# Optimization experiments

Measured on AMD Instinct MI355X. Metric: run time of the kernel, lower is better.

Reference implementation:

```python
import jax, jax.numpy as jnp
import numpy as np

B, N, E = 16, 2048, 256


def setup_inputs() -> dict:
    key = jax.random.key(0)
    ks = jax.random.split(key, 9)
    locs = jax.random.uniform(ks[0], (B, N, 2), dtype=jnp.float32)
    probe = jax.random.randint(ks[1], (B, N), 0, 2).astype(bool)
    probe = probe.at[:, 0].set(True)  # guarantee >=1 probe per instance
    s = 0.02
    W_node = jax.random.normal(ks[2], (2, E), dtype=jnp.float32) * s
    b_node = jax.random.normal(ks[3], (E,), dtype=jnp.float32) * s
    W_dist = jax.random.normal(ks[4], (1, E), dtype=jnp.float32) * s
    b_dist = jax.random.normal(ks[5], (E,), dtype=jnp.float32) * s
    W_out = jax.random.normal(ks[6], (2 * E, E), dtype=jnp.float32) * s
    b_out = jax.random.normal(ks[7], (E,), dtype=jnp.float32) * s
    return {
        "locs": locs, "probe": probe,
        "W_node": W_node, "b_node": b_node,
        "W_dist": W_dist, "b_dist": b_dist,
        "W_out": W_out, "b_out": b_out,
    }


def _cdist(x):
    # pairwise euclidean distance [B,N,N] with safe sqrt (0-grad at 0)
    sq = jnp.sum(x * x, axis=-1)                       # [B,N]
    d2 = sq[:, :, None] + sq[:, None, :] - 2.0 * jnp.einsum("bnd,bmd->bnm", x, x)
    d2 = jnp.maximum(d2, 0.0)
    pos = d2 > 0.0
    return jnp.where(pos, jnp.sqrt(jnp.where(pos, d2, 1.0)), 0.0)


def reference(locs, probe, W_node, b_node, W_dist, b_dist, W_out, b_out):
    node_emb = locs @ W_node + b_node                  # [B,N,E]
    dist = _cdist(locs)                                # [B,N,N]
    # rows i that are NOT probes are set to +inf, then min over rows (dim=1)
    dist = jnp.where(probe[:, :, None], dist, jnp.inf)
    min_dist = jnp.min(dist, axis=1)                   # [B,N] dist to nearest probe
    dist_emb = min_dist[..., None] @ W_dist + b_dist   # [B,N,E]
    cat = jnp.concatenate([node_emb, dist_emb], axis=-1)
    return cat @ W_out + b_out                         # [B,N,E]
```

## Files before the change

kernel.cpp:

```cpp
#include <hip/hip_runtime.h>

#define BSZ  16
#define NPTS 2048
#define EDIM 256
#define QB   64
#define FPB  16


__global__ __launch_bounds__(256) void prep(
    const float* __restrict__ Wn,
    const float* __restrict__ bn,
    const float* __restrict__ Wd,
    const float* __restrict__ bd,
    const float* __restrict__ Wo,
    const float* __restrict__ locs,
    const int*   __restrict__ probe,
    float*  __restrict__ partials,
    int*    __restrict__ gcnt,
    float2* __restrict__ glist)
{
    __shared__ int cnt;
    const int t   = threadIdx.x;
    const int blk = blockIdx.x;

    if (blk < FPB) {
        const int e = t;
        float a = 0.f, b = 0.f, c = 0.f, d = 0.f;
#pragma unroll
        for (int kk = 0; kk < EDIM / FPB; ++kk) {
            const int k = blk * (EDIM / FPB) + kk;
            const float wt = Wo[k * EDIM + e];
            const float wb = Wo[(EDIM + k) * EDIM + e];
            a = fmaf(Wn[k],        wt, a);
            b = fmaf(Wn[EDIM + k], wt, b);
            d = fmaf(bn[k],        wt, d);
            c = fmaf(Wd[k],        wb, c);
            d = fmaf(bd[k],        wb, d);
        }
        float* o = partials + blk * 4 * EDIM;
        o[0 * EDIM + e] = a;
        o[1 * EDIM + e] = b;
        o[2 * EDIM + e] = c;
        o[3 * EDIM + e] = d;
    } else {
        const int b = blk - FPB;
        if (t == 0) cnt = 0;
        __syncthreads();
        const float2* lb = reinterpret_cast<const float2*>(locs) + (size_t)b * NPTS;
        float2* gl = glist + (size_t)b * NPTS;
        const int lane = t & 63;
#pragma unroll
        for (int jj = 0; jj < NPTS / 256; ++jj) {
            const int j = jj * 256 + t;
            const float2 p = lb[j];
            const bool pred = probe[b * NPTS + j] != 0;
            const unsigned long long mb = __ballot(pred);
            const int rank = __popcll(mb & ((1ull << lane) - 1ull));
            int base = 0;
            if (lane == 0) base = atomicAdd(&cnt, __popcll(mb));
            base = __shfl(base, 0);
            if (pred) gl[base + rank] = p;
        }
        __syncthreads();
        if (t == 0) gcnt[b] = cnt;
    }
}

__global__ __launch_bounds__(256) void mdpp_main(
    const float*  __restrict__ locs,
    const float*  __restrict__ partials,
    const int*    __restrict__ gcnt,
    const float2* __restrict__ glist,
    const float*  __restrict__ bo,
    float*        __restrict__ out)
{
    __shared__ __align__(16) float2 pl[NPTS + 32];
    __shared__ float folded[4 * EDIM];
    __shared__ float partmin[16][QB];
    __shared__ float xq[QB], yq[QB], dq[QB];

    const int t    = threadIdx.x;
    const int bid  = blockIdx.x;
    const int b    = bid >> 5;
    const int n0   = (bid & 31) * QB;
    const int lane = t & 63;
    const int w    = t >> 6;

    const int M  = gcnt[b];
    const int Mp = (M + 31) & ~31;

    const float2* gl = glist + (size_t)b * NPTS;
    for (int i = t; i < M; i += 256) pl[i] = gl[i];
    if (t < Mp - M) pl[M + t] = make_float2(1.0e19f, 1.0e19f);

#pragma unroll
    for (int v = 0; v < 4; ++v) {
        float s = 0.f;
#pragma unroll
        for (int p = 0; p < FPB; ++p) s += partials[p * 4 * EDIM + v * EDIM + t];
        if (v == 3) s += bo[t];
        folded[v * EDIM + t] = s;
    }

    if (t < QB) {
        const float2 p = reinterpret_cast<const float2*>(locs)[(size_t)b * NPTS + n0 + t];
        xq[t] = p.x;
        yq[t] = p.y;
    }
    __syncthreads();

    const int qb    = lane & 15;
    const int chunk = w * 4 + (lane >> 4);
    float qx[4], qy[4], best[4];
#pragma unroll
    for (int j = 0; j < 4; ++j) {
        qx[j] = xq[j * 16 + qb];
        qy[j] = yq[j * 16 + qb];
        best[j] = 3.0e38f;
    }
    const int S2 = Mp >> 5;
    const float4* pl4 = reinterpret_cast<const float4*>(pl);
    const int lo = chunk * S2, hi = lo + S2;
#pragma unroll 2
    for (int i = lo; i < hi; ++i) {
        const float4 pp = pl4[i];
#pragma unroll
        for (int j = 0; j < 4; ++j) {
            const float dx0 = qx[j] - pp.x, dy0 = qy[j] - pp.y;
            const float dx1 = qx[j] - pp.z, dy1 = qy[j] - pp.w;
            best[j] = fminf(best[j], fmaf(dy0, dy0, dx0 * dx0));
            best[j] = fminf(best[j], fmaf(dy1, dy1, dx1 * dx1));
        }
    }
#pragma unroll
    for (int j = 0; j < 4; ++j) partmin[chunk][j * 16 + qb] = best[j];
    __syncthreads();

    if (t < QB) {
        float m = partmin[0][t];
#pragma unroll
        for (int c = 1; c < 16; ++c) m = fminf(m, partmin[c][t]);
        dq[t] = sqrtf(m);
    }
    __syncthreads();

    const int e0 = lane * 4;
    float A[4], Bv[4], C[4], D[4];
#pragma unroll
    for (int i = 0; i < 4; ++i) {
        A[i]  = folded[0 * EDIM + e0 + i];
        Bv[i] = folded[1 * EDIM + e0 + i];
        C[i]  = folded[2 * EDIM + e0 + i];
        D[i]  = folded[3 * EDIM + e0 + i];
    }
#pragma unroll
    for (int it = 0; it < 16; ++it) {
        const int r = it * 4 + w;
        const float xx = xq[r], yy = yq[r], dd = dq[r];
        float4 st;
        st.x = fmaf(xx, A[0], fmaf(yy, Bv[0], fmaf(dd, C[0], D[0])));
        st.y = fmaf(xx, A[1], fmaf(yy, Bv[1], fmaf(dd, C[1], D[1])));
        st.z = fmaf(xx, A[2], fmaf(yy, Bv[2], fmaf(dd, C[2], D[2])));
        st.w = fmaf(xx, A[3], fmaf(yy, Bv[3], fmaf(dd, C[3], D[3])));
        *reinterpret_cast<float4*>(
            out + ((size_t)(b * NPTS + n0 + r) * EDIM + e0)) = st;
    }
}

extern "C" void kernel_launch(void* const* d_in, const int* in_sizes, int n_in,
                              void* d_out, int out_size, void* d_ws, size_t ws_size,
                              hipStream_t stream) {
    const float* locs  = (const float*)d_in[0];
    const int*   probe = (const int*)d_in[1];
    const float* Wn = (const float*)d_in[2];
    const float* bn = (const float*)d_in[3];
    const float* Wd = (const float*)d_in[4];
    const float* bd = (const float*)d_in[5];
    const float* Wo = (const float*)d_in[6];
    const float* bo = (const float*)d_in[7];
    float* out = (float*)d_out;

    float*  partials = (float*)d_ws;
    int*    gcnt     = (int*)((char*)d_ws + 65536);
    float2* glist    = (float2*)((char*)d_ws + 65792);

    prep<<<2 * FPB, 256, 0, stream>>>(Wn, bn, Wd, bd, Wo, locs, probe,
                                      partials, gcnt, glist);
    mdpp_main<<<BSZ * (NPTS / QB), 256, 0, stream>>>(locs, partials, gcnt,
                                                     glist, bo, out);
}
```

Before: 90.90 us.

## Fuse probe compaction into main kernel and expand squared-distance algebra

Removes the separate probe-compaction blocks from the prep kernel and has every main block compact its batch's probe points into shared memory itself, storing x, y and |p|^2. The inner min loop uses the expanded form |p|^2 - 2 q·p (two FMAs per pair) and adds |q|^2 after the reduction, with interleaved float4 reads across quads. This cuts a global round-trip and shortens the dependency between kernels, but repeats the compaction 32 times per batch and may be less accurate because of cancellation in the expanded form.

```diff
diff --git a/kernel.cpp b/kernel.cpp
--- a/kernel.cpp
+++ b/kernel.cpp
@@ -6,78 +6,47 @@
 #define QB   64
 #define FPB  16
 
-
-__global__ __launch_bounds__(256) void prep(
+__global__ __launch_bounds__(256) void fold_part(
     const float* __restrict__ Wn,
     const float* __restrict__ bn,
     const float* __restrict__ Wd,
     const float* __restrict__ bd,
     const float* __restrict__ Wo,
-    const float* __restrict__ locs,
-    const int*   __restrict__ probe,
-    float*  __restrict__ partials,
-    int*    __restrict__ gcnt,
-    float2* __restrict__ glist)
+    float* __restrict__ ws)
 {
-    __shared__ int cnt;
-    const int t   = threadIdx.x;
+    const int e   = threadIdx.x;
     const int blk = blockIdx.x;
-
-    if (blk < FPB) {
-        const int e = t;
-        float a = 0.f, b = 0.f, c = 0.f, d = 0.f;
+    float a = 0.f, b = 0.f, c = 0.f, d = 0.f;
 #pragma unroll
-        for (int kk = 0; kk < EDIM / FPB; ++kk) {
-            const int k = blk * (EDIM / FPB) + kk;
-            const float wt = Wo[k * EDIM + e];
-            const float wb = Wo[(EDIM + k) * EDIM + e];
-            a = fmaf(Wn[k],        wt, a);
-            b = fmaf(Wn[EDIM + k], wt, b);
-            d = fmaf(bn[k],        wt, d);
-            c = fmaf(Wd[k],        wb, c);
-            d = fmaf(bd[k],        wb, d);
-        }
-        float* o = partials + blk * 4 * EDIM;
-        o[0 * EDIM + e] = a;
-        o[1 * EDIM + e] = b;
-        o[2 * EDIM + e] = c;
-        o[3 * EDIM + e] = d;
-    } else {
-        const int b = blk - FPB;
-        if (t == 0) cnt = 0;
-        __syncthreads();
-        const float2* lb = reinterpret_cast<const float2*>(locs) + (size_t)b * NPTS;
-        float2* gl = glist + (size_t)b * NPTS;
-        const int lane = t & 63;
-#pragma unroll
-        for (int jj = 0; jj < NPTS / 256; ++jj) {
-            const int j = jj * 256 + t;
-            const float2 p = lb[j];
-            const bool pred = probe[b * NPTS + j] != 0;
-            const unsigned long long mb = __ballot(pred);
-            const int rank = __popcll(mb & ((1ull << lane) - 1ull));
-            int base = 0;
-            if (lane == 0) base = atomicAdd(&cnt, __popcll(mb));
-            base = __shfl(base, 0);
-            if (pred) gl[base + rank] = p;
-        }
-        __syncthreads();
-        if (t == 0) gcnt[b] = cnt;
+    for (int kk = 0; kk < EDIM / FPB; ++kk) {
+        const int k = blk * (EDIM / FPB) + kk;
+        const float wt = Wo[k * EDIM + e];
+        const float wb = Wo[(EDIM + k) * EDIM + e];
+        a = fmaf(Wn[k],        wt, a);
+        b = fmaf(Wn[EDIM + k], wt, b);
+        d = fmaf(bn[k],        wt, d);
+        c = fmaf(Wd[k],        wb, c);
+        d = fmaf(bd[k],        wb, d);
     }
+    float* o = ws + blk * 4 * EDIM;
+    o[0 * EDIM + e] = a;
+    o[1 * EDIM + e] = b;
+    o[2 * EDIM + e] = c;
+    o[3 * EDIM + e] = d;
 }
 
 __global__ __launch_bounds__(256) void mdpp_main(
-    const float*  __restrict__ locs,
-    const float*  __restrict__ partials,
-    const int*    __restrict__ gcnt,
-    const float2* __restrict__ glist,
-    const float*  __restrict__ bo,
-    float*        __restrict__ out)
+    const float* __restrict__ locs,
+    const int*   __restrict__ probe,
+    const float* __restrict__ partials,
+    const float* __restrict__ bo,
+    float*       __restrict__ out)
 {
-    __shared__ __align__(16) float2 pl[NPTS + 32];
+    __shared__ __align__(16) float4 pl[NPTS + 16];
     __shared__ float folded[4 * EDIM];
     __shared__ float partmin[16][QB];
-    __shared__ float xq[QB], yq[QB], dq[QB];
+    __shared__ float xq[QB], yq[QB], sq[QB], dq[QB];
+    __shared__ int   cnt;
 
     const int t    = threadIdx.x;
     const int bid  = blockIdx.x;
@@ -85,62 +54,87 @@
     const int n0   = (bid & 31) * QB;
     const int lane = t & 63;
     const int w    = t >> 6;
+    const int quad = lane >> 4;
+    const int ql   = lane & 15;
 
-    const int M  = gcnt[b];
-    const int Mp = (M + 31) & ~31;
+    if (t == 0) cnt = 0;
 
-    const float2* gl = glist + (size_t)b * NPTS;
-    for (int i = t; i < M; i += 256) pl[i] = gl[i];
-    if (t < Mp - M) pl[M + t] = make_float2(1.0e19f, 1.0e19f);
-
+    {
+        float s0 = 0.f, s1 = 0.f, s2 = 0.f, s3 = 0.f;
 #pragma unroll
-    for (int v = 0; v < 4; ++v) {
-        float s = 0.f;
-#pragma unroll
-        for (int p = 0; p < FPB; ++p) s += partials[p * 4 * EDIM + v * EDIM + t];
-        if (v == 3) s += bo[t];
-        folded[v * EDIM + t] = s;
+        for (int p = 0; p < FPB; ++p) {
+            const float* pp = partials + p * 4 * EDIM;
+            s0 += pp[0 * EDIM + t];
+            s1 += pp[1 * EDIM + t];
+            s2 += pp[2 * EDIM + t];
+            s3 += pp[3 * EDIM + t];
+        }
+        folded[0 * EDIM + t] = s0;
+        folded[1 * EDIM + t] = s1;
+        folded[2 * EDIM + t] = s2;
+        folded[3 * EDIM + t] = s3 + bo[t];
     }
 
+    const float2* lb = reinterpret_cast<const float2*>(locs) + (size_t)b * NPTS;
+
     if (t < QB) {
-        const float2 p = reinterpret_cast<const float2*>(locs)[(size_t)b * NPTS + n0 + t];
+        const float2 p = lb[n0 + t];
         xq[t] = p.x;
         yq[t] = p.y;
+        sq[t] = fmaf(p.x, p.x, p.y * p.y);
     }
     __syncthreads();
 
-    const int qb    = lane & 15;
-    const int chunk = w * 4 + (lane >> 4);
-    float qx[4], qy[4], best[4];
+#pragma unroll
+    for (int jj = 0; jj < NPTS / 256; ++jj) {
+        const int j = jj * 256 + t;
+        const float2 p = lb[j];
+        const bool pred = probe[b * NPTS + j] != 0;
+        const unsigned long long mb = __ballot(pred);
+        const int rank = __popcll(mb & ((1ull << lane) - 1ull));
+        int base = 0;
+        if (lane == 0) base = atomicAdd(&cnt, __popcll(mb));
+        base = __shfl(base, 0);
+        if (pred) pl[base + rank] =
+            make_float4(p.x, p.y, fmaf(p.x, p.x, p.y * p.y), 0.f);
+    }
+    __syncthreads();
+
+    const int M  = cnt;
+    const int Mp = (M + 15) & ~15;
+    if (t < Mp - M) pl[M + t] = make_float4(0.f, 0.f, 1.0e19f, 0.f);
+    __syncthreads();
+
+    const int Q4   = Mp >> 2;
+    const int it_n = Q4 >> 2;
+    const float4* base4 = pl + w * Q4 + quad;
+    float ax[4], ay[4], bm[4];
 #pragma unroll
     for (int j = 0; j < 4; ++j) {
-        qx[j] = xq[j * 16 + qb];
-        qy[j] = yq[j * 16 + qb];
-        best[j] = 3.0e38f;
+        const int q = j * 16 + ql;
+        ax[j] = -2.0f * xq[q];
+        ay[j] = -2.0f * yq[q];
+        bm[j] = 3.0e38f;
     }
-    const int S2 = Mp >> 5;
-    const float4* pl4 = reinterpret_cast<const float4*>(pl);
-    const int lo = chunk * S2, hi = lo + S2;
-#pragma unroll 2
-    for (int i = lo; i < hi; ++i) {
-        const float4 pp = pl4[i];
+#pragma unroll 4
+    for (int i = 0; i < it_n; ++i) {
+        const float4 pp = base4[i * 4];
 #pragma unroll
         for (int j = 0; j < 4; ++j) {
-            const float dx0 = qx[j] - pp.x, dy0 = qy[j] - pp.y;
-            const float dx1 = qx[j] - pp.z, dy1 = qy[j] - pp.w;
-            best[j] = fminf(best[j], fmaf(dy0, dy0, dx0 * dx0));
-            best[j] = fminf(best[j], fmaf(dy1, dy1, dx1 * dx1));
+            float d2 = fmaf(ax[j], pp.x, pp.z);
+            d2 = fmaf(ay[j], pp.y, d2);
+            bm[j] = fminf(bm[j], d2);
         }
     }
 #pragma unroll
-    for (int j = 0; j < 4; ++j) partmin[chunk][j * 16 + qb] = best[j];
+    for (int j = 0; j < 4; ++j) partmin[w * 4 + quad][j * 16 + ql] = bm[j];
     __syncthreads();
 
     if (t < QB) {
         float m = partmin[0][t];
 #pragma unroll
         for (int c = 1; c < 16; ++c) m = fminf(m, partmin[c][t]);
-        dq[t] = sqrtf(m);
+        dq[t] = sqrtf(fmaxf(m + sq[t], 0.f));
     }
     __syncthreads();
 
@@ -180,12 +174,9 @@
     const float* bo = (const float*)d_in[7];
     float* out = (float*)d_out;
 
-    float*  partials = (float*)d_ws;
-    int*    gcnt     = (int*)((char*)d_ws + 65536);
-    float2* glist    = (float2*)((char*)d_ws + 65792);
+    float* partials = (float*)d_ws;
 
-    prep<<<2 * FPB, 256, 0, stream>>>(Wn, bn, Wd, bd, Wo, locs, probe,
-                                      partials, gcnt, glist);
-    mdpp_main<<<BSZ * (NPTS / QB), 256, 0, stream>>>(locs, partials, gcnt,
-                                                     glist, bo, out);
+    fold_part<<<FPB, 256, 0, stream>>>(Wn, bn, Wd, bd, Wo, partials);
+    mdpp_main<<<BSZ * (NPTS / QB), 256, 0, stream>>>(locs, probe, partials,
+                                                     bo, out);
 }
```

After: 89.61 us. No clear change (-1.4%).
